# Kernel optimization log

Measured on AMD Instinct MI355X. Metric: run time of the kernel, lower is better.

## Reference

```python
import jax, jax.numpy as jnp
import numpy as np

EPS = 1e-5


def _grid_edges(H, W):
    # radius_graph on the HxW integer grid with r=1.0, loop=False -> 4-neighbors,
    # then GCNConv's gcn_norm adds self-loops; we append them here once.
    idx = np.arange(H * W).reshape(H, W)
    r_s, r_d = idx[:, :-1].ravel(), idx[:, 1:].ravel()
    d_s, d_d = idx[:-1, :].ravel(), idx[1:, :].ravel()
    loop = np.arange(H * W)
    src = np.concatenate([r_s, r_d, d_s, d_d, loop])
    dst = np.concatenate([r_d, r_s, d_d, d_s, loop])
    return jnp.asarray(src, jnp.int32), jnp.asarray(dst, jnp.int32)


def _gcn_conv(x, W, b, src, dst, deg, dinv):
    # GCNConv(aggr='mean'): xw = x @ W; message = dinv[src]*dinv[dst] * xw[src];
    # mean-aggregate over incoming edges (incl. self-loop); add bias.
    xw = x @ W  # [B, N, Cout]
    w = (dinv[src] * dinv[dst])[None, :, None]
    agg = jnp.zeros((x.shape[0], x.shape[1], W.shape[1]), xw.dtype).at[:, dst].add(xw[:, src] * w)
    return agg / deg[None, :, None] + b


def _bn(x, gamma, beta):
    # BatchNorm2d, training-mode batch statistics (torch default), biased variance
    mu = x.mean(axis=(0, 2, 3), keepdims=True)
    var = ((x - mu) ** 2).mean(axis=(0, 2, 3), keepdims=True)
    return (x - mu) * jax.lax.rsqrt(var + EPS) * gamma[None, :, None, None] + beta[None, :, None, None]


def setup_inputs() -> dict:
    key = jax.random.key(0)
    ks = jax.random.split(key, 5)
    B, H, W, Cin, Cout = 8, 64, 64, 512, 512
    s = 0.02
    return {
        'x': jax.random.normal(ks[0], (B, H * W, Cin), jnp.float32),
        'H': H, 'W': W,
        'w_res': jax.random.normal(ks[1], (Cin, Cout), jnp.float32) * s,
        'w_pre': jax.random.normal(ks[2], (Cin, Cout), jnp.float32) * s,
        'b_pre': jnp.zeros((Cout,), jnp.float32),
        'w_g1': jax.random.normal(ks[3], (Cout, Cout), jnp.float32) * s,
        'b_g1': jnp.zeros((Cout,), jnp.float32),
        'w_g2': jax.random.normal(ks[4], (Cout, Cout), jnp.float32) * s,
        'b_g2': jnp.zeros((Cout,), jnp.float32),
        'g1': jnp.ones((Cout,), jnp.float32), 'beta1': jnp.zeros((Cout,), jnp.float32),
        'g2': jnp.ones((Cout,), jnp.float32), 'beta2': jnp.zeros((Cout,), jnp.float32),
    }


def reference(x, H, W, w_res, w_pre, b_pre, w_g1, b_g1, w_g2, b_g2, g1, beta1, g2, beta2):
    B, N, Cin = x.shape
    src, dst = _grid_edges(H, W)
    deg = jnp.zeros((N,), x.dtype).at[dst].add(1.0)  # in-degree incl. self-loops
    dinv = jax.lax.rsqrt(deg)
    # 1x1 convs on tokens == per-node matmuls
    residual = jnp.einsum('bnc,cd->bnd', x, w_res)
    xr = jnp.einsum('bnc,cd->bnd', x, w_pre) + b_pre
    h = jax.nn.relu(_gcn_conv(xr, w_g1, b_g1, src, dst, deg, dinv))
    h = jax.nn.relu(_gcn_conv(h, w_g2, b_g2, src, dst, deg, dinv))
    pooled = h.mean(axis=1)  # global_mean_pool -> [B, Cout]
    xg = _bn(pooled[:, :, None, None], g1, beta1)  # [B, Cout, 1, 1]
    res_img = residual.transpose(0, 2, 1).reshape(B, -1, H, W)
    return _bn(res_img + xg, g2, beta2)  # [B, Cout, H, W]
```

## Files before the change

kernel.cpp:

```cpp
#include <hip/hip_runtime.h>
#include <hip/hip_bf16.h>

using bf16 = __hip_bfloat16;
typedef __attribute__((ext_vector_type(8))) __bf16 bf16x8;
typedef __attribute__((ext_vector_type(4))) float f32x4;

__device__ __forceinline__ float bf2f(bf16 v) { return __bfloat162float(v); }
__device__ __forceinline__ bf16 f2bf(float f) { return __float2bfloat16(f); }

union bfu8 { bf16x8 v; bf16 h[8]; int4 i; };

__device__ __forceinline__ bool probeF32(const unsigned* probe) {
    return probe != nullptr && probe[0] == 0x3F800000u;
}
__device__ __forceinline__ float ldIn(const void* p, int i, bool f32) {
    return f32 ? ((const float*)p)[i] : bf2f(((const bf16*)p)[i]);
}

#define BATCH 8
#define GRID 64
#define NNODE 4096
#define CDIM 512
#define MROWS 32768
#define EPSBN 1e-5f

#define BM 128
#define BN 128
#define BK 32

__device__ __forceinline__ void gload16(bf16* lds, const bf16* g) {
    __builtin_amdgcn_global_load_lds(
        (const __attribute__((address_space(1))) unsigned int*)g,
        (__attribute__((address_space(3))) unsigned int*)lds, 16, 0, 0);
}

__global__ __launch_bounds__(256) void gemm_lds(const bf16* __restrict__ A,
                                                const bf16* __restrict__ BT,
                                                bf16* __restrict__ C0,
                                                bf16* __restrict__ C1,
                                                const void* __restrict__ bias,
                                                const unsigned* __restrict__ probe,
                                                int K)
{
    __shared__ __align__(16) bf16 lA[BM * BK];
    __shared__ __align__(16) bf16 lB[BN * BK];

    const bool pf32 = probeF32(probe);
    const int tid  = threadIdx.x;
    const int bm = blockIdx.x, bn = blockIdx.y;
    const int wave = tid >> 6, lane = tid & 63;
    const int wr = (wave >> 1) * 64, wc = (wave & 1) * 64;
    const int lrow = lane & 15, quad = lane >> 4;

    f32x4 acc[4][4] = {};

    const bf16* Abase = A  + (size_t)bm * BM * K;
    const bf16* Bbase = BT + (size_t)bn * BN * K;

    const int srow = wave * 32 + (lane >> 2);
    const int scol = (lane & 3) * 8;
    bf16* ldsA0 = &lA[wave * 1024];
    bf16* ldsA1 = &lA[wave * 1024 + 512];
    bf16* ldsB0 = &lB[wave * 1024];
    bf16* ldsB1 = &lB[wave * 1024 + 512];

    for (int k0 = 0; k0 < K; k0 += BK) {
        gload16(ldsA0, Abase + (size_t)srow * K + k0 + scol);
        gload16(ldsA1, Abase + (size_t)(srow + 16) * K + k0 + scol);
        gload16(ldsB0, Bbase + (size_t)srow * K + k0 + scol);
        gload16(ldsB1, Bbase + (size_t)(srow + 16) * K + k0 + scol);
        __syncthreads();

        bf16x8 af[4], bv[4];
        #pragma unroll
        for (int i = 0; i < 4; ++i)
            af[i] = *(const bf16x8*)(&lA[(wr + i * 16 + lrow) * BK + quad * 8]);
        #pragma unroll
        for (int j = 0; j < 4; ++j)
            bv[j] = *(const bf16x8*)(&lB[(wc + j * 16 + lrow) * BK + quad * 8]);

        #pragma unroll
        for (int i = 0; i < 4; ++i)
            #pragma unroll
            for (int j = 0; j < 4; ++j)
                acc[i][j] = __builtin_amdgcn_mfma_f32_16x16x32_bf16(af[i], bv[j], acc[i][j], 0, 0, 0);
        __syncthreads();
    }

    #pragma unroll
    for (int i = 0; i < 4; ++i) {
        const int mbase = bm * BM + wr + i * 16 + quad * 4;
        #pragma unroll
        for (int j = 0; j < 4; ++j) {
            int n = bn * BN + wc + j * 16 + lrow;
            bf16* Cd = C0;
            float bvv = 0.0f;
            if (C1 != nullptr && n >= CDIM) { Cd = C1; n -= CDIM; }
            else if (bias != nullptr)       { bvv = ldIn(bias, n, pf32); }
            #pragma unroll
            for (int rr = 0; rr < 4; ++rr)
                Cd[(size_t)(mbase + rr) * CDIM + n] = f2bf(acc[i][j][rr] + bvv);
        }
    }
}

__global__ __launch_bounds__(256) void convertX(const void* __restrict__ x,
                                                bf16* __restrict__ xb,
                                                const unsigned* __restrict__ probe)
{
    const bool f32 = probeF32(probe);
    const size_t i = ((size_t)blockIdx.x * 256 + threadIdx.x) * 8;
    if (f32) {
        const float4 u0 = *(const float4*)((const float*)x + i);
        const float4 u1 = *(const float4*)((const float*)x + i + 4);
        bf16 t[8] = { f2bf(u0.x), f2bf(u0.y), f2bf(u0.z), f2bf(u0.w),
                      f2bf(u1.x), f2bf(u1.y), f2bf(u1.z), f2bf(u1.w) };
        *(int4*)(xb + i) = *(const int4*)t;
    } else {
        *(int4*)(xb + i) = *(const int4*)((const bf16*)x + i);
    }
}

__global__ __launch_bounds__(256) void transpose512(const void* __restrict__ src,
                                                    bf16* __restrict__ dst,
                                                    const unsigned* __restrict__ probe)
{
    __shared__ float tile[64][65];
    const bool f32 = probeF32(probe);
    const int bx = blockIdx.x, by = blockIdx.y;
    const int t = threadIdx.x;
    const int col = t & 63, rbase = t >> 6;
    #pragma unroll 4
    for (int i = 0; i < 16; ++i) {
        int r = i * 4 + rbase;
        tile[r][col] = ldIn(src, (by * 64 + r) * 512 + bx * 64 + col, f32);
    }
    __syncthreads();
    #pragma unroll 4
    for (int i = 0; i < 16; ++i) {
        int r = i * 4 + rbase;
        dst[(size_t)(bx * 64 + r) * 512 + by * 64 + col] = f2bf(tile[col][r]);
    }
}

__device__ __forceinline__ float degOf(int y, int x) {
    return 1.0f + (y > 0) + (y < GRID - 1) + (x > 0) + (x < GRID - 1);
}

__global__ __launch_bounds__(256) void gcn_agg_v2(const bf16* __restrict__ T,
                                                  const void* __restrict__ bias,
                                                  const unsigned* __restrict__ probe,
                                                  bf16* __restrict__ H)
{
    const bool f32 = probeF32(probe);
    const int t = threadIdx.x;
    const int lane = t & 63, sub = t >> 6;
    const int n = blockIdx.x * 4 + sub;
    const int b = blockIdx.y;
    const int y = n >> 6, x = n & 63;
    const int cg = lane * 8;

    const float deg = degOf(y, x);
    const float dn  = rsqrtf(deg);
    const float inv = dn / deg;

    const bf16* cptr = T + ((size_t)b * NNODE + n) * CDIM + cg;

    bfu8 vc; vc.v = *(const bf16x8*)cptr;
    float s[8];
    #pragma unroll
    for (int j = 0; j < 8; ++j) s[j] = dn * bf2f(vc.h[j]);

    if (y > 0)        { float d = rsqrtf(degOf(y - 1, x)); bfu8 u; u.v = *(const bf16x8*)(cptr - 64 * CDIM);
                        #pragma unroll
                        for (int j = 0; j < 8; ++j) s[j] += d * bf2f(u.h[j]); }
    if (y < GRID - 1) { float d = rsqrtf(degOf(y + 1, x)); bfu8 u; u.v = *(const bf16x8*)(cptr + 64 * CDIM);
                        #pragma unroll
                        for (int j = 0; j < 8; ++j) s[j] += d * bf2f(u.h[j]); }
    if (x > 0)        { float d = rsqrtf(degOf(y, x - 1)); bfu8 u; u.v = *(const bf16x8*)(cptr - CDIM);
                        #pragma unroll
                        for (int j = 0; j < 8; ++j) s[j] += d * bf2f(u.h[j]); }
    if (x < GRID - 1) { float d = rsqrtf(degOf(y, x + 1)); bfu8 u; u.v = *(const bf16x8*)(cptr + CDIM);
                        #pragma unroll
                        for (int j = 0; j < 8; ++j) s[j] += d * bf2f(u.h[j]); }

    bfu8 o;
    #pragma unroll
    for (int j = 0; j < 8; ++j)
        o.h[j] = f2bf(fmaxf(s[j] * inv + ldIn(bias, cg + j, f32), 0.0f));
    *(int4*)(H + ((size_t)b * NNODE + n) * CDIM + cg) = o.i;
}

__global__ __launch_bounds__(256) void gcn_agg_pool_v3(const bf16* __restrict__ T,
                                                       const void* __restrict__ bias,
                                                       const unsigned* __restrict__ probe,
                                                       float* __restrict__ poolPart)
{
    const bool f32 = probeF32(probe);
    const int y = blockIdx.x;
    const int b = blockIdx.y;
    const int t = threadIdx.x;
    const int lane = t & 63, sub = t >> 6;
    const int cg = lane * 8;

    const bf16* base = T + (size_t)b * NNODE * CDIM;

    float biasv[8];
    #pragma unroll
    for (int j = 0; j < 8; ++j) biasv[j] = ldIn(bias, cg + j, f32);

    float acc[8] = {};

    for (int xi = 0; xi < 16; ++xi) {
        const int x = sub * 16 + xi;
        const int n = y * 64 + x;
        const float deg = degOf(y, x);
        const float dn  = rsqrtf(deg);
        const float inv = dn / deg;
        const bf16* cptr = base + (size_t)n * CDIM + cg;

        bfu8 vc; vc.v = *(const bf16x8*)cptr;
        float s[8];
        #pragma unroll
        for (int j = 0; j < 8; ++j) s[j] = dn * bf2f(vc.h[j]);

        if (y > 0)        { float d = rsqrtf(degOf(y - 1, x)); bfu8 u; u.v = *(const bf16x8*)(cptr - 64 * CDIM);
                            #pragma unroll
                            for (int j = 0; j < 8; ++j) s[j] += d * bf2f(u.h[j]); }
        if (y < GRID - 1) { float d = rsqrtf(degOf(y + 1, x)); bfu8 u; u.v = *(const bf16x8*)(cptr + 64 * CDIM);
                            #pragma unroll
                            for (int j = 0; j < 8; ++j) s[j] += d * bf2f(u.h[j]); }
        if (x > 0)        { float d = rsqrtf(degOf(y, x - 1)); bfu8 u; u.v = *(const bf16x8*)(cptr - CDIM);
                            #pragma unroll
                            for (int j = 0; j < 8; ++j) s[j] += d * bf2f(u.h[j]); }
        if (x < GRID - 1) { float d = rsqrtf(degOf(y, x + 1)); bfu8 u; u.v = *(const bf16x8*)(cptr + CDIM);
                            #pragma unroll
                            for (int j = 0; j < 8; ++j) s[j] += d * bf2f(u.h[j]); }

        #pragma unroll
        for (int j = 0; j < 8; ++j)
            acc[j] += fmaxf(s[j] * inv + biasv[j], 0.0f);
    }

    __shared__ float red[4][64][9];
    #pragma unroll
    for (int j = 0; j < 8; ++j) red[sub][lane][j] = acc[j];
    __syncthreads();
    if (sub == 0) {
        float* dst = poolPart + (size_t)(b * GRID + y) * CDIM + cg;
        #pragma unroll
        for (int j = 0; j < 8; ++j)
            dst[j] = red[0][lane][j] + red[1][lane][j] + red[2][lane][j] + red[3][lane][j];
    }
}

__global__ void bn1_kernel(const float* __restrict__ poolPart,
                           const void* __restrict__ g1, const void* __restrict__ beta1,
                           const unsigned* __restrict__ probe,
                           float* __restrict__ xg)
{
    const bool f32 = probeF32(probe);
    const int c = blockIdx.x * 256 + threadIdx.x;
    float p[BATCH];
    float mu = 0.0f;
    #pragma unroll
    for (int b = 0; b < BATCH; ++b) {
        float a0 = 0, a1 = 0, a2 = 0, a3 = 0;
        const float* src = poolPart + (size_t)b * GRID * CDIM + c;
        #pragma unroll 4
        for (int y = 0; y < GRID; y += 4) {
            a0 += src[(size_t)(y + 0) * CDIM];
            a1 += src[(size_t)(y + 1) * CDIM];
            a2 += src[(size_t)(y + 2) * CDIM];
            a3 += src[(size_t)(y + 3) * CDIM];
        }
        p[b] = (a0 + a1 + a2 + a3) * (1.0f / (float)NNODE);
        mu += p[b];
    }
    mu *= (1.0f / (float)BATCH);
    float var = 0.0f;
    #pragma unroll
    for (int b = 0; b < BATCH; ++b) { float d = p[b] - mu; var += d * d; }
    var *= (1.0f / (float)BATCH);
    const float rs = rsqrtf(var + EPSBN) * ldIn(g1, c, f32);
    const float bt = ldIn(beta1, c, f32);
    #pragma unroll
    for (int b = 0; b < BATCH; ++b)
        xg[b * CDIM + c] = (p[b] - mu) * rs + bt;
}

__global__ __launch_bounds__(256) void bn2_stats_part(const bf16* __restrict__ R,
                                                      const float* __restrict__ xg,
                                                      float* __restrict__ bn2Part)
{
    const int t = threadIdx.x;
    const int lane = t & 63, sub = t >> 6;
    const int cg = lane * 8;
    const int row0 = blockIdx.x * 128;
    const int b = row0 >> 12;

    float xgv[8];
    #pragma unroll
    for (int j = 0; j < 8; ++j) xgv[j] = xg[b * CDIM + cg + j];

    float s[8] = {}, q[8] = {};
    #pragma unroll
    for (int i0 = 0; i0 < 4; ++i0) {
        const bf16* base = R + (size_t)(row0 + i0 * 32 + sub * 8) * CDIM + cg;
        #pragma unroll
        for (int k = 0; k < 8; ++k) {
            bfu8 u; u.v = *(const bf16x8*)(base + (size_t)k * CDIM);
            #pragma unroll
            for (int j = 0; j < 8; ++j) {
                float v = bf2f(u.h[j]) + xgv[j];
                s[j] += v; q[j] += v * v;
            }
        }
    }

    __shared__ float redS[4][64][9], redQ[4][64][9];
    #pragma unroll
    for (int j = 0; j < 8; ++j) { redS[sub][lane][j] = s[j]; redQ[sub][lane][j] = q[j]; }
    __syncthreads();
    if (sub == 0) {
        float* dst = bn2Part + (size_t)blockIdx.x * 1024;
        #pragma unroll
        for (int j = 0; j < 8; ++j) {
            dst[cg + j]       = redS[0][lane][j] + redS[1][lane][j] + redS[2][lane][j] + redS[3][lane][j];
            dst[512 + cg + j] = redQ[0][lane][j] + redQ[1][lane][j] + redQ[2][lane][j] + redQ[3][lane][j];
        }
    }
}

__global__ void bn2_reduce(const float* __restrict__ bn2Part, float* __restrict__ sums)
{
    const int c = blockIdx.x * 256 + threadIdx.x;
    float a0 = 0, a1 = 0, a2 = 0, a3 = 0, a4 = 0, a5 = 0, a6 = 0, a7 = 0;
    #pragma unroll 4
    for (int blk = 0; blk < 256; blk += 8) {
        a0 += bn2Part[(size_t)(blk + 0) * 1024 + c];
        a1 += bn2Part[(size_t)(blk + 1) * 1024 + c];
        a2 += bn2Part[(size_t)(blk + 2) * 1024 + c];
        a3 += bn2Part[(size_t)(blk + 3) * 1024 + c];
        a4 += bn2Part[(size_t)(blk + 4) * 1024 + c];
        a5 += bn2Part[(size_t)(blk + 5) * 1024 + c];
        a6 += bn2Part[(size_t)(blk + 6) * 1024 + c];
        a7 += bn2Part[(size_t)(blk + 7) * 1024 + c];
    }
    sums[c] = ((a0 + a1) + (a2 + a3)) + ((a4 + a5) + (a6 + a7));
}

__global__ void bn2_final(const float* __restrict__ sums, const float* __restrict__ xg,
                          const void* __restrict__ g2, const void* __restrict__ beta2,
                          const unsigned* __restrict__ probe,
                          float* __restrict__ scale, float* __restrict__ tshift)
{
    const bool f32 = probeF32(probe);
    const int c = blockIdx.x * 256 + threadIdx.x;
    const float mu  = sums[c] * (1.0f / (float)MROWS);
    const float var = sums[512 + c] * (1.0f / (float)MROWS) - mu * mu;
    const float sc  = ldIn(g2, c, f32) * rsqrtf(var + EPSBN);
    scale[c] = sc;
    const float base = ldIn(beta2, c, f32) - mu * sc;
    #pragma unroll
    for (int b = 0; b < BATCH; ++b)
        tshift[b * CDIM + c] = xg[b * CDIM + c] * sc + base;
}

__global__ __launch_bounds__(256) void out_transpose(const bf16* __restrict__ R,
                                                     const float* __restrict__ scale,
                                                     const float* __restrict__ tshift,
                                                     const unsigned* __restrict__ probe,
                                                     void* __restrict__ outv)
{
    __shared__ float tile[64][65];
    const bool f32 = probeF32(probe);
    const int nt = blockIdx.x;
    const int ct = blockIdx.y;
    const int b  = blockIdx.z;
    const int t = threadIdx.x;
    const int c0 = ct * 64, n0 = nt * 64;

    const int rr  = t >> 3;
    const int cch = (t & 7) * 8;
    #pragma unroll
    for (int half = 0; half < 2; ++half) {
        int r = rr + half * 32;
        bfu8 u; u.v = *(const bf16x8*)(R + ((size_t)(b * NNODE + n0 + r)) * CDIM + c0 + cch);
        #pragma unroll
        for (int j = 0; j < 8; ++j) tile[r][cch + j] = bf2f(u.h[j]);
    }
    __syncthreads();

    const int col = t & 63, rbase = t >> 6;
    if (f32) {
        float* out = (float*)outv;
        #pragma unroll 4
        for (int i = 0; i < 16; ++i) {
            int cc = i * 4 + rbase;
            float sc  = scale[c0 + cc];
            float tsh = tshift[b * CDIM + c0 + cc];
            out[((size_t)(b * CDIM + c0 + cc)) * NNODE + n0 + col] = tile[col][cc] * sc + tsh;
        }
    } else {
        bf16* out = (bf16*)outv;
        #pragma unroll 4
        for (int i = 0; i < 16; ++i) {
            int cc = i * 4 + rbase;
            float sc  = scale[c0 + cc];
            float tsh = tshift[b * CDIM + c0 + cc];
            out[((size_t)(b * CDIM + c0 + cc)) * NNODE + n0 + col] = f2bf(tile[col][cc] * sc + tsh);
        }
    }
}

extern "C" void kernel_launch(void* const* d_in, const int* in_sizes, int n_in,
                              void* d_out, int out_size, void* d_ws, size_t ws_size,
                              hipStream_t stream)
{
    const void* x     = d_in[0];
    const void* w_res = d_in[3];
    const void* w_pre = d_in[4];
    const void* b_pre = d_in[5];
    const void* b_g1  = d_in[7];
    const void* w_g1  = d_in[6];
    const void* w_g2  = d_in[8];
    const void* b_g2  = d_in[9];
    const void* g1    = d_in[10];
    const void* beta1 = d_in[11];
    const void* g2    = d_in[12];
    const void* beta2 = d_in[13];
    const unsigned* probe = (const unsigned*)g1;

    char* ws = (char*)d_ws;
    constexpr size_t WSZ = (size_t)512 * 512 * 2;

    bf16* BTpre = (bf16*)(ws);
    bf16* BTres = (bf16*)(ws + WSZ);
    bf16* BTg1  = (bf16*)(ws + 2 * WSZ);
    bf16* BTg2  = (bf16*)(ws + 3 * WSZ);
    char* smallb = ws + 4 * WSZ;
    float* sums   = (float*)(smallb);
    float* xg     = (float*)(smallb + 4096);
    float* scale  = (float*)(smallb + 4096 + 16384);
    float* tshift = (float*)(smallb + 4096 + 16384 + 2048);
    bf16* Rres = (bf16*)(smallb + 65536);

    char* dA = (char*)d_out;
    char* dB = (char*)d_out + (size_t)MROWS * CDIM * 2;

    bf16* XR = (bf16*)dA;
    bf16* Tt = (bf16*)dB;
    float* poolPart = (float*)dA;
    float* bn2Part  = (float*)(dA + (1 << 20));

    {
        dim3 g(8, 8), blk(256);
        transpose512<<<g, blk, 0, stream>>>(w_pre, BTpre, probe);
        transpose512<<<g, blk, 0, stream>>>(w_res, BTres, probe);
        transpose512<<<g, blk, 0, stream>>>(w_g1, BTg1, probe);
        transpose512<<<g, blk, 0, stream>>>(w_g2, BTg2, probe);
    }

    dim3 blk(256);
    convertX<<<dim3(MROWS * CDIM / (256 * 8)), blk, 0, stream>>>(x, Tt, probe);
    gemm_lds<<<dim3(MROWS / BM, 1024 / BN), blk, 0, stream>>>(Tt, BTpre, XR, Rres, b_pre, probe, CDIM);
    gemm_lds<<<dim3(MROWS / BM, CDIM / BN), blk, 0, stream>>>(XR, BTg1, Tt, nullptr, nullptr, nullptr, CDIM);
    gcn_agg_v2<<<dim3(NNODE / 4, BATCH), blk, 0, stream>>>(Tt, b_g1, probe, XR);
    gemm_lds<<<dim3(MROWS / BM, CDIM / BN), blk, 0, stream>>>(XR, BTg2, Tt, nullptr, nullptr, nullptr, CDIM);
    gcn_agg_pool_v3<<<dim3(GRID, BATCH), blk, 0, stream>>>(Tt, b_g2, probe, poolPart);
    bn1_kernel<<<dim3(2), blk, 0, stream>>>(poolPart, g1, beta1, probe, xg);
    bn2_stats_part<<<dim3(MROWS / 128), blk, 0, stream>>>(Rres, xg, bn2Part);
    bn2_reduce<<<dim3(4), blk, 0, stream>>>(bn2Part, sums);
    bn2_final<<<dim3(2), blk, 0, stream>>>(sums, xg, g2, beta2, probe, scale, tshift);
    out_transpose<<<dim3(NNODE / 64, CDIM / 64, BATCH), blk, 0, stream>>>(Rres, scale, tshift, probe, d_out);
}
```

Measured before the change: 421.1 us.

## Double-buffer GEMM LDS tiles and merge weight transposes into one launch

```diff
diff --git a/kernel.cpp b/kernel.cpp
--- a/kernel.cpp
+++ b/kernel.cpp
@@ -33,6 +33,8 @@
         (const __attribute__((address_space(1))) unsigned int*)g,
         (__attribute__((address_space(3))) unsigned int*)lds, 16, 0, 0);
 }
+
+#define PIN() __builtin_amdgcn_sched_barrier(0)
 
 __global__ __launch_bounds__(256) void gemm_lds(const bf16* __restrict__ A,
                                                 const bf16* __restrict__ BT,
@@ -42,8 +44,8 @@
                                                 const unsigned* __restrict__ probe,
                                                 int K)
 {
-    __shared__ __align__(16) bf16 lA[BM * BK];
-    __shared__ __align__(16) bf16 lB[BN * BK];
+    __shared__ __align__(16) bf16 lA[2][BM * BK];
+    __shared__ __align__(16) bf16 lB[2][BN * BK];
 
     const bool pf32 = probeF32(probe);
     const int tid  = threadIdx.x;
@@ -59,33 +61,67 @@
 
     const int srow = wave * 32 + (lane >> 2);
     const int scol = (lane & 3) * 8;
-    bf16* ldsA0 = &lA[wave * 1024];
-    bf16* ldsA1 = &lA[wave * 1024 + 512];
-    bf16* ldsB0 = &lB[wave * 1024];
-    bf16* ldsB1 = &lB[wave * 1024 + 512];
-
-    for (int k0 = 0; k0 < K; k0 += BK) {
-        gload16(ldsA0, Abase + (size_t)srow * K + k0 + scol);
-        gload16(ldsA1, Abase + (size_t)(srow + 16) * K + k0 + scol);
-        gload16(ldsB0, Bbase + (size_t)srow * K + k0 + scol);
-        gload16(ldsB1, Bbase + (size_t)(srow + 16) * K + k0 + scol);
-        __syncthreads();
-
-        bf16x8 af[4], bv[4];
-        #pragma unroll
-        for (int i = 0; i < 4; ++i)
-            af[i] = *(const bf16x8*)(&lA[(wr + i * 16 + lrow) * BK + quad * 8]);
-        #pragma unroll
-        for (int j = 0; j < 4; ++j)
-            bv[j] = *(const bf16x8*)(&lB[(wc + j * 16 + lrow) * BK + quad * 8]);
-
-        #pragma unroll
-        for (int i = 0; i < 4; ++i)
-            #pragma unroll
-            for (int j = 0; j < 4; ++j)
-                acc[i][j] = __builtin_amdgcn_mfma_f32_16x16x32_bf16(af[i], bv[j], acc[i][j], 0, 0, 0);
-        __syncthreads();
-    }
+    const bf16* gA0 = Abase + (size_t)srow * K + scol;
+    const bf16* gA1 = Abase + (size_t)(srow + 16) * K + scol;
+    const bf16* gB0 = Bbase + (size_t)srow * K + scol;
+    const bf16* gB1 = Bbase + (size_t)(srow + 16) * K + scol;
+    bf16* laBase = &lA[0][0];
+    bf16* lbBase = &lB[0][0];
+    const int wofs = wave * 1024;
+
+#define STAGE(BUF, TILE) do {                                              \
+        const size_t koff_ = (size_t)(TILE) * BK;                          \
+        gload16(laBase + (BUF) * (BM * BK) + wofs,       gA0 + koff_);     \
+        gload16(laBase + (BUF) * (BM * BK) + wofs + 512, gA1 + koff_);     \
+        gload16(lbBase + (BUF) * (BN * BK) + wofs,       gB0 + koff_);     \
+        gload16(lbBase + (BUF) * (BN * BK) + wofs + 512, gB1 + koff_);     \
+    } while (0)
+
+#define COMPUTE(BUF) do {                                                  \
+        const bf16* pA_ = laBase + (BUF) * (BM * BK);                      \
+        const bf16* pB_ = lbBase + (BUF) * (BN * BK);                      \
+        bf16x8 af[4], bv[4];                                               \
+        _Pragma("unroll")                                                  \
+        for (int i = 0; i < 4; ++i)                                        \
+            af[i] = *(const bf16x8*)(pA_ + (wr + i * 16 + lrow) * BK + quad * 8); \
+        _Pragma("unroll")                                                  \
+        for (int j = 0; j < 4; ++j)                                        \
+            bv[j] = *(const bf16x8*)(pB_ + (wc + j * 16 + lrow) * BK + quad * 8); \
+        _Pragma("unroll")                                                  \
+        for (int i = 0; i < 4; ++i)                                        \
+            _Pragma("unroll")                                              \
+            for (int j = 0; j < 4; ++j)                                    \
+                acc[i][j] = __builtin_amdgcn_mfma_f32_16x16x32_bf16(af[i], bv[j], acc[i][j], 0, 0, 0); \
+    } while (0)
+
+    const int NT = K / BK;
+
+    STAGE(0, 0);
+    int t = 0;
+    for (; t + 3 < NT; t += 2) {
+        STAGE(1, t + 1);
+        asm volatile("s_waitcnt vmcnt(4)" ::: "memory");
+        __builtin_amdgcn_s_barrier(); PIN();
+        COMPUTE(0);
+        PIN(); __builtin_amdgcn_s_barrier(); PIN();
+
+        STAGE(0, t + 2);
+        asm volatile("s_waitcnt vmcnt(4)" ::: "memory");
+        __builtin_amdgcn_s_barrier(); PIN();
+        COMPUTE(1);
+        PIN(); __builtin_amdgcn_s_barrier(); PIN();
+    }
+    STAGE(1, t + 1);
+    asm volatile("s_waitcnt vmcnt(4)" ::: "memory");
+    __builtin_amdgcn_s_barrier(); PIN();
+    COMPUTE(0);
+    PIN(); __builtin_amdgcn_s_barrier(); PIN();
+    asm volatile("s_waitcnt vmcnt(0)" ::: "memory");
+    __builtin_amdgcn_s_barrier(); PIN();
+    COMPUTE(1);
+
+#undef STAGE
+#undef COMPUTE
 
     #pragma unroll
     for (int i = 0; i < 4; ++i) {
@@ -121,12 +157,18 @@
     }
 }
 
-__global__ __launch_bounds__(256) void transpose512(const void* __restrict__ src,
-                                                    bf16* __restrict__ dst,
-                                                    const unsigned* __restrict__ probe)
+__global__ __launch_bounds__(256) void transpose512x4(const void* __restrict__ s0,
+                                                      const void* __restrict__ s1,
+                                                      const void* __restrict__ s2,
+                                                      const void* __restrict__ s3,
+                                                      bf16* __restrict__ dstBase,
+                                                      const unsigned* __restrict__ probe)
 {
     __shared__ float tile[64][65];
     const bool f32 = probeF32(probe);
+    const int z = blockIdx.z;
+    const void* src = (z == 0) ? s0 : (z == 1) ? s1 : (z == 2) ? s2 : s3;
+    bf16* dst = dstBase + (size_t)z * 512 * 512;
     const int bx = blockIdx.x, by = blockIdx.y;
     const int t = threadIdx.x;
     const int col = t & 63, rbase = t >> 6;
@@ -422,8 +464,8 @@
     const void* w_res = d_in[3];
     const void* w_pre = d_in[4];
     const void* b_pre = d_in[5];
+    const void* w_g1  = d_in[6];
     const void* b_g1  = d_in[7];
-    const void* w_g1  = d_in[6];
     const void* w_g2  = d_in[8];
     const void* b_g2  = d_in[9];
     const void* g1    = d_in[10];
@@ -436,7 +478,6 @@
     constexpr size_t WSZ = (size_t)512 * 512 * 2;
 
     bf16* BTpre = (bf16*)(ws);
-    bf16* BTres = (bf16*)(ws + WSZ);
     bf16* BTg1  = (bf16*)(ws + 2 * WSZ);
     bf16* BTg2  = (bf16*)(ws + 3 * WSZ);
     char* smallb = ws + 4 * WSZ;
@@ -454,13 +495,8 @@
     float* poolPart = (float*)dA;
     float* bn2Part  = (float*)(dA + (1 << 20));
 
-    {
-        dim3 g(8, 8), blk(256);
-        transpose512<<<g, blk, 0, stream>>>(w_pre, BTpre, probe);
-        transpose512<<<g, blk, 0, stream>>>(w_res, BTres, probe);
-        transpose512<<<g, blk, 0, stream>>>(w_g1, BTg1, probe);
-        transpose512<<<g, blk, 0, stream>>>(w_g2, BTg2, probe);
-    }
+    transpose512x4<<<dim3(8, 8, 4), 256, 0, stream>>>(w_pre, w_res, w_g1, w_g2,
+                                                      BTpre, probe);
 
     dim3 blk(256);
     convertX<<<dim3(MROWS * CDIM / (256 * 8)), blk, 0, stream>>>(x, Tt, probe);
```

After: 397.8 us. 5.5% less time.
